# Performance work log

Measured on AMD Instinct MI355X. Metric: run time of the kernel, lower is better.

Reference implementation:

```python
import jax, jax.numpy as jnp
import numpy as np

B, T, P, C, H = 2, 2048, 2048, 1024, 16  # batch, new tokens, cached tokens, n_embd, n_head
HD = C // H  # head_dim = 64


def setup_inputs() -> dict:
    key = jax.random.key(0)
    ks = jax.random.split(key, 5)
    return {
        "x": jax.random.normal(ks[0], (B, T, C), dtype=jnp.float32),
        "k_cache": jax.random.normal(ks[1], (B, P, C), dtype=jnp.float32),
        "v_cache": jax.random.normal(ks[2], (B, P, C), dtype=jnp.float32),
        "W_attn": jax.random.normal(ks[3], (C, 3 * C), dtype=jnp.float32) * 0.02,
        "W_proj": jax.random.normal(ks[4], (C, C), dtype=jnp.float32) * 0.02,
    }


def reference(x, k_cache, v_cache, W_attn, W_proj):
    # c_attn (no bias): qkv projection, then split into q, k_rem, v_rem
    qkv = x @ W_attn                      # [B, T, 3C]
    q, k_rem, v_rem = jnp.split(qkv, 3, axis=2)
    # KV-cache concat along time
    k_full = jnp.concatenate([k_cache, k_rem], axis=1)  # [B, S, C], S = P + T
    v_full = jnp.concatenate([v_cache, v_rem], axis=1)
    S = P + T
    # reshape to heads
    qh = q.reshape(B, T, H, HD).transpose(0, 2, 1, 3)       # [B, H, T, HD]
    kh = k_full.reshape(B, S, H, HD).transpose(0, 2, 1, 3)  # [B, H, S, HD]
    vh = v_full.reshape(B, S, H, HD).transpose(0, 2, 1, 3)  # [B, H, S, HD]
    # full attention matrix (module explicitly disables flash)
    att = jnp.einsum("bhqd,bhkd->bhqk", qh, kh) * (1.0 / np.sqrt(HD))  # [B,H,T,S]
    # cache-offset causal mask: query global position = P + i attends to key j <= P + i
    mask = jnp.arange(S)[None, :] <= (P + jnp.arange(T))[:, None]  # [T, S]
    att = jnp.where(mask[None, None], att, -jnp.inf)
    att = jax.nn.softmax(att, axis=-1)
    # dropout p=0.0 (inference) -> no-op
    y = jnp.einsum("bhqk,bhkd->bhqd", att, vh)  # [B, H, T, HD]
    y = y.transpose(0, 2, 1, 3).reshape(B, T, C)
    y = y @ W_proj  # c_proj, no bias; resid dropout p=0 -> no-op
    return (y, k_full, v_full)
```

## Files before the change

kernel.cpp:

```cpp
#include <hip/hip_runtime.h>

#define BB 2
#define TT 2048
#define PP 2048
#define CC 1024
#define HH 16
#define SS 4096

typedef unsigned short u16;
typedef __attribute__((ext_vector_type(8))) short s16x8;
typedef __attribute__((ext_vector_type(4))) float f32x4;
typedef __attribute__((ext_vector_type(4))) unsigned short u16x4;

#define QSCALE 0.18033688011112042f

__device__ __forceinline__ u16 f2bf(float f) {
  unsigned u = __float_as_uint(f);
  u += 0x7fff + ((u >> 16) & 1);
  return (u16)(u >> 16);
}

__global__ __launch_bounds__(256) void cvt_f32_bf16(const float* __restrict__ src,
                                                    u16* __restrict__ dst) {
  size_t i = ((size_t)blockIdx.x * 256 + threadIdx.x) * 4;
  f32x4 v = *(const f32x4*)(src + i);
  u16x4 o = { f2bf(v[0]), f2bf(v[1]), f2bf(v[2]), f2bf(v[3]) };
  *(u16x4*)(dst + i) = o;
}

__global__ __launch_bounds__(256) void transpose_w_bf16(const float* __restrict__ src,
                                                        u16* __restrict__ dst,
                                                        int rows, int cols) {
  __shared__ float tile[64][65];
  int r0 = blockIdx.y * 64, c0 = blockIdx.x * 64;
  int tx = threadIdx.x & 63, ty = threadIdx.x >> 6;
#pragma unroll
  for (int i = 0; i < 16; i++) {
    int r = ty + i * 4;
    tile[r][tx] = src[(size_t)(r0 + r) * cols + c0 + tx];
  }
  __syncthreads();
#pragma unroll
  for (int i = 0; i < 16; i++) {
    int cc = ty + i * 4;
    dst[(size_t)(c0 + cc) * rows + r0 + tx] = f2bf(tile[tx][cc]);
  }
}

__global__ __launch_bounds__(256) void cache_copy(const float* __restrict__ kc,
                                                  const float* __restrict__ vc,
                                                  float* __restrict__ kf,
                                                  float* __restrict__ vf,
                                                  u16* __restrict__ kb) {
  size_t flat = ((size_t)blockIdx.x * 256 + threadIdx.x) * 4;
  int b = (int)(flat >> 21);
  size_t dsto = flat + (size_t)b * (TT * CC);
  f32x4 kv = *(const f32x4*)(kc + flat);
  f32x4 vv = *(const f32x4*)(vc + flat);
  *(f32x4*)(kf + dsto) = kv;
  *(f32x4*)(vf + dsto) = vv;
  u16x4 k4 = { f2bf(kv[0]), f2bf(kv[1]), f2bf(kv[2]), f2bf(kv[3]) };
  *(u16x4*)(kb + dsto) = k4;
}

__global__ __launch_bounds__(256) void vT_cache_kernel(const float* __restrict__ vc,
                                                       u16* __restrict__ vTb) {
  __shared__ float tile[64][65];
  int bh = blockIdx.y, b = bh >> 4, h = bh & 15;
  int p0 = blockIdx.x * 64;
  int tx = threadIdx.x & 63, ty = threadIdx.x >> 6;
#pragma unroll
  for (int i = 0; i < 16; i++) {
    int p = ty + i * 4;
    tile[p][tx] = vc[(size_t)(b * PP + p0 + p) * CC + h * 64 + tx];
  }
  __syncthreads();
#pragma unroll
  for (int i = 0; i < 16; i++) {
    int d = ty + i * 4;
    vTb[(size_t)((b * HH + h) * 64 + d) * SS + p0 + tx] = f2bf(tile[tx][d]);
  }
}

__global__ __launch_bounds__(256) void vT_rem_kernel(const float* __restrict__ vf,
                                                     u16* __restrict__ vTb) {
  __shared__ float tile[64][65];
  int bh = blockIdx.y, b = bh >> 4, h = bh & 15;
  int p0 = blockIdx.x * 64;
  int tx = threadIdx.x & 63, ty = threadIdx.x >> 6;
#pragma unroll
  for (int i = 0; i < 16; i++) {
    int p = ty + i * 4;
    tile[p][tx] = vf[(size_t)(b * SS + PP + p0 + p) * CC + h * 64 + tx];
  }
  __syncthreads();
#pragma unroll
  for (int i = 0; i < 16; i++) {
    int d = ty + i * 4;
    vTb[(size_t)((b * HH + h) * 64 + d) * SS + PP + p0 + tx] = f2bf(tile[tx][d]);
  }
}

__global__ __launch_bounds__(256) void gemm_bt(const u16* __restrict__ A,
                                               const u16* __restrict__ BT,
                                               int N, int mode,
                                               float* __restrict__ out0,
                                               u16* __restrict__ qb,
                                               float* __restrict__ kf,
                                               u16* __restrict__ kb,
                                               float* __restrict__ vf) {
  __shared__ u16 As[128 * 72];
  __shared__ u16 Bs[128 * 72];
  const int m0 = blockIdx.y * 128, n0 = blockIdx.x * 128;
  const int tid = threadIdx.x, lane = tid & 63, wave = tid >> 6;
  const int wm = wave & 1, wn = wave >> 1;
  const int c = lane & 15, quad = lane >> 4;
  const int chunk = tid & 7, rp = tid >> 3;

  f32x4 acc[4][4] = {};

  for (int k0 = 0; k0 < 1024; k0 += 64) {
#pragma unroll
    for (int it = 0; it < 4; it++) {
      int r = it * 32 + rp;
      *(s16x8*)&As[r * 72 + chunk * 8] =
          *(const s16x8*)(A + (size_t)(m0 + r) * 1024 + k0 + chunk * 8);
      *(s16x8*)&Bs[r * 72 + chunk * 8] =
          *(const s16x8*)(BT + (size_t)(n0 + r) * 1024 + k0 + chunk * 8);
    }
    __syncthreads();
#pragma unroll
    for (int kc = 0; kc < 64; kc += 32) {
      s16x8 af[4], bf[4];
#pragma unroll
      for (int i = 0; i < 4; i++) {
        af[i] = *(const s16x8*)&As[(wm * 64 + i * 16 + c) * 72 + kc + quad * 8];
        bf[i] = *(const s16x8*)&Bs[(wn * 64 + i * 16 + c) * 72 + kc + quad * 8];
      }
#pragma unroll
      for (int mi = 0; mi < 4; mi++)
#pragma unroll
        for (int ni = 0; ni < 4; ni++)
          acc[mi][ni] = __builtin_amdgcn_mfma_f32_16x16x32_bf16(af[mi], bf[ni], acc[mi][ni], 0, 0, 0);
    }
    __syncthreads();
  }

#pragma unroll
  for (int mi = 0; mi < 4; mi++) {
#pragma unroll
    for (int ni = 0; ni < 4; ni++) {
      f32x4 v = acc[mi][ni];
      int gmb = m0 + wm * 64 + mi * 16 + quad * 4;
      int gn = n0 + wn * 64 + ni * 16 + c;
      if (mode == 0) {
#pragma unroll
        for (int r = 0; r < 4; r++)
          out0[(size_t)(gmb + r) * N + gn] = v[r];
      } else {
        int region = n0 >> 10;
        if (region == 0) {
#pragma unroll
          for (int r = 0; r < 4; r++)
            qb[(size_t)(gmb + r) * 1024 + gn] = f2bf(v[r] * QSCALE);
        } else if (region == 1) {
          int ccol = gn - 1024;
#pragma unroll
          for (int r = 0; r < 4; r++) {
            int gm = gmb + r, b = gm >> 11, t = gm & 2047;
            size_t off = (size_t)b * (SS * CC) + (size_t)(PP + t) * CC + ccol;
            kf[off] = v[r];
            kb[off] = f2bf(v[r]);
          }
        } else {
          int ccol = gn - 2048;
#pragma unroll
          for (int r = 0; r < 4; r++) {
            int gm = gmb + r, b = gm >> 11, t = gm & 2047;
            vf[(size_t)b * (SS * CC) + (size_t)(PP + t) * CC + ccol] = v[r];
          }
        }
      }
    }
  }
}

__global__ __launch_bounds__(512, 4) void attn_kernel(const u16* __restrict__ qb,
                                                      const u16* __restrict__ kb,
                                                      const u16* __restrict__ vT,
                                                      u16* __restrict__ yb) {
  __shared__ u16 Ks[64 * 72];
  __shared__ u16 Vs[80 * 72];
  __shared__ u16 Ps[8][16 * 72];
  const int bh = blockIdx.y, b = bh >> 4, h = bh & 15;
  const int qt = gridDim.x - 1 - blockIdx.x;
  const int q0 = qt * 128;
  const int tid = threadIdx.x, lane = tid & 63, wave = tid >> 6;
  const int c = lane & 15, quad = lane >> 4;
  const int chunk = tid & 7, rp = tid >> 3;

  const int s_end = PP + q0 + 128;

  const u16* kptr = kb + (size_t)(b * SS + rp) * 1024 + h * 64 + chunk * 8;
  const u16* vptr = vT + (size_t)((b * HH + h) * 64 + rp) * SS + chunk * 8;

  s16x8 kreg = *(const s16x8*)kptr;
  s16x8 vreg = *(const s16x8*)vptr;

  for (int i = tid; i < 16 * 72; i += 512)
    Vs[64 * 72 + i] = (i < 72) ? (u16)0x3F80 : (u16)0;
  __syncthreads();
  const s16x8 ones0 = *(const s16x8*)&Vs[(64 + c) * 72 + quad * 8];
  const s16x8 ones1 = *(const s16x8*)&Vs[(64 + c) * 72 + 32 + quad * 8];

  s16x8 qf[2];
  {
    int qr = q0 + wave * 16 + c;
    qf[0] = *(const s16x8*)(qb + (size_t)(b * TT + qr) * 1024 + h * 64 + quad * 8);
    qf[1] = *(const s16x8*)(qb + (size_t)(b * TT + qr) * 1024 + h * 64 + 32 + quad * 8);
  }

  f32x4 o[5] = {};
  float m = -1e30f;
  u16* Pw = Ps[wave];

  for (int s0 = 0; s0 < s_end; s0 += 64) {
    *(s16x8*)&Ks[rp * 72 + chunk * 8] = kreg;
    *(s16x8*)&Vs[rp * 72 + chunk * 8] = vreg;
    __syncthreads();

    if (s0 + 64 < s_end) {
      kptr += 64 * 1024;
      vptr += 64;
      kreg = *(const s16x8*)kptr;
      vreg = *(const s16x8*)vptr;
    }

    f32x4 sc[4];
    __builtin_amdgcn_s_setprio(1);
#pragma unroll
    for (int nt = 0; nt < 4; nt++) {
      s16x8 kf0 = *(const s16x8*)&Ks[(nt * 16 + c) * 72 + quad * 8];
      s16x8 kf1 = *(const s16x8*)&Ks[(nt * 16 + c) * 72 + 32 + quad * 8];
      f32x4 z = { 0.f, 0.f, 0.f, 0.f };
      z = __builtin_amdgcn_mfma_f32_16x16x32_bf16(qf[0], kf0, z, 0, 0, 0);
      z = __builtin_amdgcn_mfma_f32_16x16x32_bf16(qf[1], kf1, z, 0, 0, 0);
      sc[nt] = z;
    }
    __builtin_amdgcn_s_setprio(0);

    const int diag = s0 - (PP + q0);
    if (diag >= 0) {
#pragma unroll
      for (int nt = 0; nt < 4; nt++) {
        int col = nt * 16 + c + diag;
#pragma unroll
        for (int r = 0; r < 4; r++) {
          int rq = wave * 16 + quad * 4 + r;
          if (col > rq) sc[nt][r] = -1e30f;
        }
      }
    }

    float lm = -1e30f;
#pragma unroll
    for (int nt = 0; nt < 4; nt++)
      lm = fmaxf(lm, fmaxf(fmaxf(sc[nt][0], sc[nt][1]),
                           fmaxf(sc[nt][2], sc[nt][3])));
#pragma unroll
    for (int off = 1; off < 64; off <<= 1)
      lm = fmaxf(lm, __shfl_xor(lm, off, 64));
    if (lm > m + 8.0f) {
      float alpha = __builtin_amdgcn_exp2f(m - lm);
      m = lm;
#pragma unroll
      for (int dt = 0; dt < 5; dt++)
#pragma unroll
        for (int r = 0; r < 4; r++) o[dt][r] *= alpha;
    }

#pragma unroll
    for (int nt = 0; nt < 4; nt++)
#pragma unroll
      for (int r = 0; r < 4; r++)
        Pw[(quad * 4 + r) * 72 + nt * 16 + c] =
            f2bf(__builtin_amdgcn_exp2f(sc[nt][r] - m));
    s16x8 pa0 = *(const s16x8*)&Pw[c * 72 + quad * 8];
    s16x8 pa1 = *(const s16x8*)&Pw[c * 72 + 32 + quad * 8];

    __builtin_amdgcn_s_setprio(1);
#pragma unroll
    for (int dt = 0; dt < 4; dt++) {
      s16x8 vb0 = *(const s16x8*)&Vs[(dt * 16 + c) * 72 + quad * 8];
      s16x8 vb1 = *(const s16x8*)&Vs[(dt * 16 + c) * 72 + 32 + quad * 8];
      o[dt] = __builtin_amdgcn_mfma_f32_16x16x32_bf16(pa0, vb0, o[dt], 0, 0, 0);
      o[dt] = __builtin_amdgcn_mfma_f32_16x16x32_bf16(pa1, vb1, o[dt], 0, 0, 0);
    }
    o[4] = __builtin_amdgcn_mfma_f32_16x16x32_bf16(pa0, ones0, o[4], 0, 0, 0);
    o[4] = __builtin_amdgcn_mfma_f32_16x16x32_bf16(pa1, ones1, o[4], 0, 0, 0);
    __builtin_amdgcn_s_setprio(0);
    __syncthreads();
  }

#pragma unroll
  for (int r = 0; r < 4; r++) {
    float l = __shfl(o[4][r], (lane & 48), 64);
    float inv = 1.0f / l;
    int qr = q0 + wave * 16 + quad * 4 + r;
#pragma unroll
    for (int dt = 0; dt < 4; dt++)
      yb[(size_t)(b * TT + qr) * 1024 + h * 64 + dt * 16 + c] = f2bf(o[dt][r] * inv);
  }
}

extern "C" void kernel_launch(void* const* d_in, const int* in_sizes, int n_in,
                              void* d_out, int out_size, void* d_ws, size_t ws_size,
                              hipStream_t stream) {
  const float* x       = (const float*)d_in[0];
  const float* k_cache = (const float*)d_in[1];
  const float* v_cache = (const float*)d_in[2];
  const float* W_attn  = (const float*)d_in[3];
  const float* W_proj  = (const float*)d_in[4];

  float* out_y = (float*)d_out;
  float* out_k = out_y + (size_t)BB * TT * CC;
  float* out_v = out_k + (size_t)BB * SS * CC;

  u16* xb  = (u16*)d_ws;
  u16* WaT = xb  + 4194304;
  u16* WpT = WaT + 3145728;
  u16* qb  = WpT + 1048576;
  u16* kb  = qb  + 4194304;
  u16* vT  = kb  + 8388608;
  u16* yb  = vT  + 8388608;

  cvt_f32_bf16<<<dim3(4096), dim3(256), 0, stream>>>(x, xb);
  transpose_w_bf16<<<dim3(48, 16), dim3(256), 0, stream>>>(W_attn, WaT, 1024, 3072);
  transpose_w_bf16<<<dim3(16, 16), dim3(256), 0, stream>>>(W_proj, WpT, 1024, 1024);
  cache_copy<<<dim3(4096), dim3(256), 0, stream>>>(k_cache, v_cache, out_k, out_v, kb);
  vT_cache_kernel<<<dim3(32, 32), dim3(256), 0, stream>>>(v_cache, vT);
  gemm_bt<<<dim3(24, 32), dim3(256), 0, stream>>>(xb, WaT, 3072, 1, nullptr, qb, out_k, kb, out_v);
  vT_rem_kernel<<<dim3(32, 32), dim3(256), 0, stream>>>(out_v, vT);
  attn_kernel<<<dim3(16, 32), dim3(512), 0, stream>>>(qb, kb, vT, yb);
  gemm_bt<<<dim3(8, 32), dim3(256), 0, stream>>>(yb, WpT, 1024, 0, out_y, nullptr, nullptr, nullptr, nullptr);
}
```

Baseline: 361.7 us.

## Double-buffer K/V tiles in attention and remap blocks by XCD

The attention kernel now double-buffers the K and V shared-memory tiles. The next tile is written into the alternate buffer after the PV MFMAs, which removes one __syncthreads per iteration. The grid is flattened to 1D and remapped so that each XCD handles a fixed group of four (batch, head) pairs, with the heaviest query tiles scheduled first, to improve L2 locality of K/V. The row-sum 'ones' operand is built in registers rather than read from shared memory, at the cost of more LDS use for the second buffer.

Measured after the change: 332.0 us. 8.2% less time.

```diff
diff --git a/kernel.cpp b/kernel.cpp
--- a/kernel.cpp
+++ b/kernel.cpp
@@ -189,11 +189,14 @@
                                                       const u16* __restrict__ kb,
                                                       const u16* __restrict__ vT,
                                                       u16* __restrict__ yb) {
-  __shared__ u16 Ks[64 * 72];
-  __shared__ u16 Vs[80 * 72];
+  __shared__ u16 Ks[2][64 * 72];
+  __shared__ u16 Vs[2][64 * 72];
   __shared__ u16 Ps[8][16 * 72];
-  const int bh = blockIdx.y, b = bh >> 4, h = bh & 15;
-  const int qt = gridDim.x - 1 - blockIdx.x;
+  const int L = blockIdx.x;
+  const int xcd = L & 7, rest = L >> 3;
+  const int qt = 15 - (rest >> 2);
+  const int bh = (xcd << 2) | (rest & 3);
+  const int b = bh >> 4, h = bh & 15;
   const int q0 = qt * 128;
   const int tid = threadIdx.x, lane = tid & 63, wave = tid >> 6;
   const int c = lane & 15, quad = lane >> 4;
@@ -204,14 +207,15 @@
   const u16* kptr = kb + (size_t)(b * SS + rp) * 1024 + h * 64 + chunk * 8;
   const u16* vptr = vT + (size_t)((b * HH + h) * 64 + rp) * SS + chunk * 8;
 
-  s16x8 kreg = *(const s16x8*)kptr;
-  s16x8 vreg = *(const s16x8*)vptr;
-
-  for (int i = tid; i < 16 * 72; i += 512)
-    Vs[64 * 72 + i] = (i < 72) ? (u16)0x3F80 : (u16)0;
-  __syncthreads();
-  const s16x8 ones0 = *(const s16x8*)&Vs[(64 + c) * 72 + quad * 8];
-  const s16x8 ones1 = *(const s16x8*)&Vs[(64 + c) * 72 + 32 + quad * 8];
+  {
+    s16x8 k0 = *(const s16x8*)kptr;
+    s16x8 v0 = *(const s16x8*)vptr;
+    *(s16x8*)&Ks[0][rp * 72 + chunk * 8] = k0;
+    *(s16x8*)&Vs[0][rp * 72 + chunk * 8] = v0;
+  }
+
+  const short ov = (c == 0) ? (short)0x3F80 : (short)0;
+  const s16x8 ones = { ov, ov, ov, ov, ov, ov, ov, ov };
 
   s16x8 qf[2];
   {
@@ -223,25 +227,29 @@
   f32x4 o[5] = {};
   float m = -1e30f;
   u16* Pw = Ps[wave];
-
-  for (int s0 = 0; s0 < s_end; s0 += 64) {
-    *(s16x8*)&Ks[rp * 72 + chunk * 8] = kreg;
-    *(s16x8*)&Vs[rp * 72 + chunk * 8] = vreg;
+  s16x8 kreg, vreg;
+
+  int cur = 0;
+  for (int s0 = 0; s0 < s_end; s0 += 64, cur ^= 1) {
     __syncthreads();
 
-    if (s0 + 64 < s_end) {
+    const bool more = (s0 + 64 < s_end);
+    if (more) {
       kptr += 64 * 1024;
       vptr += 64;
       kreg = *(const s16x8*)kptr;
       vreg = *(const s16x8*)vptr;
     }
 
+    const u16* Kc = Ks[cur];
+    const u16* Vc = Vs[cur];
+
     f32x4 sc[4];
     __builtin_amdgcn_s_setprio(1);
 #pragma unroll
     for (int nt = 0; nt < 4; nt++) {
-      s16x8 kf0 = *(const s16x8*)&Ks[(nt * 16 + c) * 72 + quad * 8];
-      s16x8 kf1 = *(const s16x8*)&Ks[(nt * 16 + c) * 72 + 32 + quad * 8];
+      s16x8 kf0 = *(const s16x8*)&Kc[(nt * 16 + c) * 72 + quad * 8];
+      s16x8 kf1 = *(const s16x8*)&Kc[(nt * 16 + c) * 72 + 32 + quad * 8];
       f32x4 z = { 0.f, 0.f, 0.f, 0.f };
       z = __builtin_amdgcn_mfma_f32_16x16x32_bf16(qf[0], kf0, z, 0, 0, 0);
       z = __builtin_amdgcn_mfma_f32_16x16x32_bf16(qf[1], kf1, z, 0, 0, 0);
@@ -291,15 +299,19 @@
     __builtin_amdgcn_s_setprio(1);
 #pragma unroll
     for (int dt = 0; dt < 4; dt++) {
-      s16x8 vb0 = *(const s16x8*)&Vs[(dt * 16 + c) * 72 + quad * 8];
-      s16x8 vb1 = *(const s16x8*)&Vs[(dt * 16 + c) * 72 + 32 + quad * 8];
+      s16x8 vb0 = *(const s16x8*)&Vc[(dt * 16 + c) * 72 + quad * 8];
+      s16x8 vb1 = *(const s16x8*)&Vc[(dt * 16 + c) * 72 + 32 + quad * 8];
       o[dt] = __builtin_amdgcn_mfma_f32_16x16x32_bf16(pa0, vb0, o[dt], 0, 0, 0);
       o[dt] = __builtin_amdgcn_mfma_f32_16x16x32_bf16(pa1, vb1, o[dt], 0, 0, 0);
     }
-    o[4] = __builtin_amdgcn_mfma_f32_16x16x32_bf16(pa0, ones0, o[4], 0, 0, 0);
-    o[4] = __builtin_amdgcn_mfma_f32_16x16x32_bf16(pa1, ones1, o[4], 0, 0, 0);
+    o[4] = __builtin_amdgcn_mfma_f32_16x16x32_bf16(pa0, ones, o[4], 0, 0, 0);
+    o[4] = __builtin_amdgcn_mfma_f32_16x16x32_bf16(pa1, ones, o[4], 0, 0, 0);
     __builtin_amdgcn_s_setprio(0);
-    __syncthreads();
+
+    if (more) {
+      *(s16x8*)&Ks[cur ^ 1][rp * 72 + chunk * 8] = kreg;
+      *(s16x8*)&Vs[cur ^ 1][rp * 72 + chunk * 8] = vreg;
+    }
   }
 
 #pragma unroll
@@ -341,6 +353,6 @@
   vT_cache_kernel<<<dim3(32, 32), dim3(256), 0, stream>>>(v_cache, vT);
   gemm_bt<<<dim3(24, 32), dim3(256), 0, stream>>>(xb, WaT, 3072, 1, nullptr, qb, out_k, kb, out_v);
   vT_rem_kernel<<<dim3(32, 32), dim3(256), 0, stream>>>(out_v, vT);
-  attn_kernel<<<dim3(16, 32), dim3(512), 0, stream>>>(qb, kb, vT, yb);
+  attn_kernel<<<dim3(512), dim3(512), 0, stream>>>(qb, kb, vT, yb);
   gemm_bt<<<dim3(8, 32), dim3(256), 0, stream>>>(yb, WpT, 1024, 0, out_y, nullptr, nullptr, nullptr, nullptr);
 }
```
